# Performance work log

Hardware: AMD Instinct MI355X
Metric: run time of the kernel (lower is better)

Reference implementation:

```python
import jax, jax.numpy as jnp
import numpy as np
import math

B, S, D, H, FF = 32, 577, 768, 12, 3072
Dh = D // H
EPS = 1e-5


def layer_norm(x, w, b):
    mu = jnp.mean(x, axis=-1, keepdims=True)
    var = jnp.mean(jnp.square(x - mu), axis=-1, keepdims=True)
    return (x - mu) * jax.lax.rsqrt(var + EPS) * w + b


def setup_inputs() -> dict:
    key = jax.random.key(0)
    ks = jax.random.split(key, 12)
    s = 0.02
    return {
        "x": jax.random.normal(ks[0], (B, S, D), dtype=jnp.float32),
        "ln1_w": jnp.ones((D,), jnp.float32),
        "ln1_b": jnp.zeros((D,), jnp.float32),
        # stacked per-head Q/K/V projections (head order matches torch concat order)
        "Wq": jax.random.normal(ks[1], (H, D, Dh), jnp.float32) * s,
        "bq": jnp.zeros((H, Dh), jnp.float32),
        "Wk": jax.random.normal(ks[2], (H, D, Dh), jnp.float32) * s,
        "bk": jnp.zeros((H, Dh), jnp.float32),
        "Wv": jax.random.normal(ks[3], (H, D, Dh), jnp.float32) * s,
        "bv": jnp.zeros((H, Dh), jnp.float32),
        "Wo": jax.random.normal(ks[4], (D, D), jnp.float32) * s,
        "bo": jnp.zeros((D,), jnp.float32),
        "ln2_w": jnp.ones((D,), jnp.float32),
        "ln2_b": jnp.zeros((D,), jnp.float32),
        "W1": jax.random.normal(ks[5], (D, FF), jnp.float32) * s,
        "b1": jnp.zeros((FF,), jnp.float32),
        "W2": jax.random.normal(ks[6], (FF, D), jnp.float32) * s,
        "b2": jnp.zeros((D,), jnp.float32),
    }


def reference(x, ln1_w, ln1_b, Wq, bq, Wk, bk, Wv, bv, Wo, bo, ln2_w, ln2_b, W1, b1, W2, b2):
    # pre-norm attention
    h = layer_norm(x, ln1_w, ln1_b)  # [B,S,D]
    q = jnp.einsum('bsd,hde->bhse', h, Wq) + bq[:, None, :]
    k = jnp.einsum('bsd,hde->bhse', h, Wk) + bk[:, None, :]
    v = jnp.einsum('bsd,hde->bhse', h, Wv) + bv[:, None, :]
    scores = jnp.einsum('bhse,bhte->bhst', q, k) / math.sqrt(Dh)
    probs = jax.nn.softmax(scores, axis=-1)
    ctx = jnp.einsum('bhst,bhte->bhse', probs, v)  # [B,H,S,Dh]
    ctx = ctx.transpose(0, 2, 1, 3).reshape(B, S, H * Dh)  # concat heads
    attn_out = ctx @ Wo + bo
    x = x + attn_out
    # pre-norm MLP (exact GELU, as nn.GELU default)
    h2 = layer_norm(x, ln2_w, ln2_b)
    mlp = jax.nn.gelu(h2 @ W1 + b1, approximate=False) @ W2 + b2
    return x + mlp
```

## Files before the change

kernel.cpp:

```cpp
#include <hip/hip_runtime.h>
#include <hip/hip_bf16.h>
#include <stdint.h>

#define B_ 32
#define S_ 577
#define D_ 768
#define H_ 12
#define FF_ 3072
#define MROWS (B_*S_)

typedef __attribute__((ext_vector_type(8))) short sh8;
typedef __attribute__((ext_vector_type(4))) float f32x4;
typedef __attribute__((ext_vector_type(4))) unsigned short us4;

static __device__ __forceinline__ unsigned short f2b(float f) {
  __hip_bfloat16 h = __float2bfloat16(f);
  return *reinterpret_cast<unsigned short*>(&h);
}
static __device__ __forceinline__ float b2f(unsigned short u) {
  __hip_bfloat16 h;
  *reinterpret_cast<unsigned short*>(&h) = u;
  return __bfloat162float(h);
}

static __device__ __forceinline__ float fast_gelu(float v) {
  const float z = fabsf(v) * 0.70710678118f;
  const float t = __builtin_amdgcn_rcpf(__builtin_fmaf(0.3275911f, z, 1.0f));
  float p = 1.061405429f;
  p = __builtin_fmaf(p, t, -1.453152027f);
  p = __builtin_fmaf(p, t,  1.421413741f);
  p = __builtin_fmaf(p, t, -0.284496736f);
  p = __builtin_fmaf(p, t,  0.254829592f);
  p = p * t;
  const float e = __expf(-z * z);
  const float erf_abs = __builtin_fmaf(-p, e, 1.0f);
  const float erf_v = copysignf(erf_abs, v);
  const float hv = 0.5f * v;
  return __builtin_fmaf(hv, erf_v, hv);
}

#define GLOAD_LDS16(gp, lp) \
  __builtin_amdgcn_global_load_lds((const __attribute__((address_space(1))) unsigned int*)(gp), \
                                   (__attribute__((address_space(3))) unsigned int*)(lp), 16, 0, 0)

__global__ __launch_bounds__(256) void packT64(
    const float* __restrict__ src, unsigned short* __restrict__ dst, int K, int N)
{
  __shared__ unsigned short t[64][65];
  const int tid = threadIdx.x;
  const int c = tid & 63, r4 = tid >> 6;
  const int kb = blockIdx.y * 64, nb = blockIdx.x * 64;
#pragma unroll
  for (int p = 0; p < 16; ++p) {
    const int ko = p * 4 + r4;
    t[c][ko] = f2b(src[(size_t)(kb + ko) * N + nb + c]);
  }
  __syncthreads();
#pragma unroll
  for (int p = 0; p < 16; ++p) {
    const int rr = p * 4 + r4;
    dst[(size_t)(nb + rr) * K + kb + c] = t[rr][c];
  }
}

__global__ __launch_bounds__(256) void packQKV64(
    const float* __restrict__ Wq, const float* __restrict__ Wk, const float* __restrict__ Wv,
    unsigned short* __restrict__ dst)
{
  __shared__ unsigned short t[64][65];
  const int tid = threadIdx.x;
  const int c = tid & 63, r4 = tid >> 6;
  const int kb = blockIdx.x * 64;
  const int h = blockIdx.y;
  const int which = blockIdx.z;
  const float* src = ((which == 0) ? Wq : (which == 1) ? Wk : Wv) + (size_t)h * 768 * 64;
  const float scl = (which == 0) ? 0.125f : 1.0f;
#pragma unroll
  for (int p = 0; p < 16; ++p) {
    const int ko = p * 4 + r4;
    t[c][ko] = f2b(src[(size_t)(kb + ko) * 64 + c] * scl);
  }
  __syncthreads();
  unsigned short* db = dst + (size_t)(which * 768 + h * 64) * 768;
#pragma unroll
  for (int p = 0; p < 16; ++p) {
    const int rr = p * 4 + r4;
    db[(size_t)rr * 768 + kb + c] = t[rr][c];
  }
}

__global__ __launch_bounds__(256) void bias_pack(
    const float* __restrict__ bq, const float* __restrict__ bk, const float* __restrict__ bv,
    float* __restrict__ biasq)
{
  const int idx = blockIdx.x * 256 + threadIdx.x;
  if (idx < 2304) {
    const int wb = idx / 768, rb = idx - wb * 768;
    const float* bb = (wb == 0) ? bq : (wb == 1) ? bk : bv;
    biasq[idx] = bb[rb] * (wb == 0 ? 0.125f : 1.0f);
  }
}

__global__ __launch_bounds__(256) void ln_bf16(
    const float* __restrict__ x, const float* __restrict__ w, const float* __restrict__ bse,
    unsigned short* __restrict__ out)
{
  const int row = blockIdx.x;
  const int tid = threadIdx.x;
  const float* xr = x + (size_t)row * 768;
  float v0 = xr[tid], v1 = xr[tid + 256], v2 = xr[tid + 512];
  float s = v0 + v1 + v2;
  float ss = v0 * v0 + v1 * v1 + v2 * v2;
#pragma unroll
  for (int off = 32; off >= 1; off >>= 1) {
    s  += __shfl_xor(s, off);
    ss += __shfl_xor(ss, off);
  }
  __shared__ float red[8];
  const int wv = tid >> 6, ln = tid & 63;
  if (ln == 0) { red[wv] = s; red[wv + 4] = ss; }
  __syncthreads();
  s  = red[0] + red[1] + red[2] + red[3];
  ss = red[4] + red[5] + red[6] + red[7];
  const float mu = s * (1.f / 768.f);
  const float var = ss * (1.f / 768.f) - mu * mu;
  const float rs = rsqrtf(var + 1e-5f);
  unsigned short* orow = out + (size_t)row * 768;
  orow[tid]       = f2b((v0 - mu) * rs * w[tid]       + bse[tid]);
  orow[tid + 256] = f2b((v1 - mu) * rs * w[tid + 256] + bse[tid + 256]);
  orow[tid + 512] = f2b((v2 - mu) * rs * w[tid + 512] + bse[tid + 512]);
}

template<int EPI>
__global__ __launch_bounds__(256, 3) void gemm128(
    const unsigned short* __restrict__ A, const unsigned short* __restrict__ Bt,
    const float* __restrict__ bias, const float* __restrict__ res,
    unsigned short* __restrict__ obf, float* __restrict__ of32,
    int M, int N, int K)
{
  __shared__ __align__(16) unsigned short sAB[2][128 * 64];
  const int tid = threadIdx.x;
  const int wid = tid >> 6, ln = tid & 63;
  const int wr = wid >> 1, wc = wid & 1;
  const int l15 = ln & 15, lg = ln >> 4;
  const int l7 = l15 & 7;
  const int uo0 = ((lg) ^ l7) * 8;
  const int uo1 = ((4 + lg) ^ l7) * 8;
  const int srow = ln >> 3;
  const int scol = ((ln & 7) ^ srow) * 8;
  const int NT = K >> 6;

  const int gx = N >> 7;
  const int gm = (M + 127) >> 7;
  const int nwg = gridDim.x;
  const int q = nwg >> 3, r = nwg & 7;
  const int x = blockIdx.x & 7, ii = blockIdx.x >> 3;
  const int wg = (x < r ? x * (q + 1) : r * (q + 1) + (x - r) * q) + ii;
  int bm, bn;
  {
    const int g8 = gx >> 3, rem = gx & 7;
    const int per_full = gm << 3;
    if (wg < g8 * per_full) {
      const int bg = wg / per_full;
      const int r2 = wg - bg * per_full;
      bm = r2 >> 3; bn = (bg << 3) + (r2 & 7);
    } else {
      const int r2 = wg - g8 * per_full;
      bm = r2 / rem; bn = (g8 << 3) + (r2 - bm * rem);
    }
  }

  const int arow = wr * 64 + l15;
  const int brow = wc * 64 + l15;

  const unsigned short* ap0; const unsigned short* ap1;
  const unsigned short* ap2; const unsigned short* ap3;
  const unsigned short* bp0; const unsigned short* bp1;
  const unsigned short* bp2; const unsigned short* bp3;
  {
    int g0 = bm * 128 + (wid * 4 + 0) * 8 + srow; if (g0 >= M) g0 = M - 1;
    int g1 = bm * 128 + (wid * 4 + 1) * 8 + srow; if (g1 >= M) g1 = M - 1;
    int g2 = bm * 128 + (wid * 4 + 2) * 8 + srow; if (g2 >= M) g2 = M - 1;
    int g3 = bm * 128 + (wid * 4 + 3) * 8 + srow; if (g3 >= M) g3 = M - 1;
    ap0 = A + (size_t)g0 * K + scol; ap1 = A + (size_t)g1 * K + scol;
    ap2 = A + (size_t)g2 * K + scol; ap3 = A + (size_t)g3 * K + scol;
    const int b0 = bn * 128 + (wid * 4 + 0) * 8 + srow;
    bp0 = Bt + (size_t)b0 * K + scol;
    bp1 = bp0 + (size_t)8 * K; bp2 = bp0 + (size_t)16 * K; bp3 = bp0 + (size_t)24 * K;
  }
  unsigned short* const lA = sAB[0] + wid * 4 * 512;
  unsigned short* const lB = sAB[1] + wid * 4 * 512;

  f32x4 acc[4][4] = {};

  for (int t = 0; t < NT; ++t) {
    __syncthreads();
    GLOAD_LDS16(ap0, lA);        GLOAD_LDS16(ap1, lA + 512);
    GLOAD_LDS16(ap2, lA + 1024); GLOAD_LDS16(ap3, lA + 1536);
    GLOAD_LDS16(bp0, lB);        GLOAD_LDS16(bp1, lB + 512);
    GLOAD_LDS16(bp2, lB + 1024); GLOAD_LDS16(bp3, lB + 1536);
    ap0 += 64; ap1 += 64; ap2 += 64; ap3 += 64;
    bp0 += 64; bp1 += 64; bp2 += 64; bp3 += 64;
    asm volatile("s_waitcnt vmcnt(0)" ::: "memory");
    __syncthreads();

#pragma unroll
    for (int kk = 0; kk < 2; ++kk) {
      const int uo = kk ? uo1 : uo0;
      sh8 af[4], bf[4];
#pragma unroll
      for (int mi = 0; mi < 4; ++mi)
        af[mi] = *(const sh8*)(sAB[0] + (arow + mi * 16) * 64 + uo);
#pragma unroll
      for (int ni = 0; ni < 4; ++ni)
        bf[ni] = *(const sh8*)(sAB[1] + (brow + ni * 16) * 64 + uo);
#pragma unroll
      for (int mi = 0; mi < 4; ++mi)
#pragma unroll
        for (int ni = 0; ni < 4; ++ni)
          acc[mi][ni] = __builtin_amdgcn_mfma_f32_16x16x32_bf16(af[mi], bf[ni], acc[mi][ni], 0, 0, 0);
    }
  }

  constexpr int ESTR = 132;
  float* eps = (float*)sAB;
  const int ecol = (tid & 31) * 4;
  const int gcol = bn * 128 + ecol;
  const f32x4 bvh = *(const f32x4*)(bias + gcol);
  const int erow0 = tid >> 5;
#pragma unroll
  for (int pass = 0; pass < 4; ++pass) {
    __syncthreads();
    if (wr == (pass >> 1)) {
      const int mib = (pass & 1) * 2;
#pragma unroll
      for (int ml = 0; ml < 2; ++ml)
#pragma unroll
        for (int ni = 0; ni < 4; ++ni)
#pragma unroll
          for (int rr = 0; rr < 4; ++rr)
            eps[(ml * 16 + lg * 4 + rr) * ESTR + wc * 64 + ni * 16 + l15] = acc[mib + ml][ni][rr];
    }
    __syncthreads();
#pragma unroll
    for (int pp = 0; pp < 4; ++pp) {
      const int rl = pp * 8 + erow0;
      const int grow = bm * 128 + pass * 32 + rl;
      if (grow < M) {
        f32x4 v = *(const f32x4*)(eps + rl * ESTR + ecol);
        v += bvh;
        if (EPI == 2) {
#pragma unroll
          for (int e = 0; e < 4; ++e) v[e] = fast_gelu(v[e]);
        }
        if (EPI == 1) {
          const f32x4 rv = *(const f32x4*)(res + (size_t)grow * N + gcol);
          v += rv;
          *(f32x4*)(of32 + (size_t)grow * N + gcol) = v;
        } else {
          us4 o = { f2b(v[0]), f2b(v[1]), f2b(v[2]), f2b(v[3]) };
          *(us4*)(obf + (size_t)grow * N + gcol) = o;
        }
      }
    }
  }
}

__global__ __launch_bounds__(512) void attn(
    const unsigned short* __restrict__ qkv, unsigned short* __restrict__ ctx)
{
  constexpr int KP = 72;
  __shared__ __align__(16) unsigned short sQ[128 * KP];
  __shared__ __align__(16) unsigned short sK[64 * KP];
  __shared__ __align__(16) unsigned short sVT[64 * KP];
  __shared__ __align__(16) unsigned short sP[8][16 * KP];
  const int tid = threadIdx.x, wv = tid >> 6, ln = tid & 63;
  const int l15 = ln & 15, lg = ln >> 4;
  const int b = blockIdx.z, h = blockIdx.y, qt = blockIdx.x;
  const size_t base = (size_t)b * S_ * 2304 + h * 64;
  const unsigned short* qp = qkv + base;
  const unsigned short* kp = qkv + base + 768;
  const unsigned short* vp = qkv + base + 1536;

  {
    const int r = tid >> 2, c = (tid & 3) * 16;
    int row = qt * 128 + r; if (row >= S_) row = S_ - 1;
    const unsigned short* g = qp + (size_t)row * 2304 + c;
    *(sh8*)(sQ + r * KP + c)     = *(const sh8*)g;
    *(sh8*)(sQ + r * KP + c + 8) = *(const sh8*)(g + 8);
  }

  const int kr = tid >> 3, kc = (tid & 7) * 8;
  const unsigned short* krow = kp + (size_t)kr * 2304 + kc;
  unsigned short* const sKdst = sK + kr * KP + kc;
  const int ve = tid & 63, vkvb = tid >> 6;
  const unsigned short* vrow = vp + (size_t)vkvb * 8 * 2304 + ve;
  unsigned short* const sVdst = sVT + ve * KP + vkvb * 8;

  f32x4 oacc[4] = {};
  float m_run = -1e30f, l_run = 0.f;
  const int nt = (S_ + 63) / 64;
  for (int t = 0; t < nt; ++t) {
    __syncthreads();
    if (t < nt - 1) {
      *(sh8*)sKdst = *(const sh8*)krow;
      krow += (size_t)64 * 2304;
      {
        unsigned short val[8];
#pragma unroll
        for (int j = 0; j < 8; ++j) val[j] = vrow[(size_t)j * 2304];
        *(sh8*)sVdst = *(sh8*)val;
        vrow += (size_t)64 * 2304;
      }
    } else {
      {
        int row = t * 64 + kr; if (row >= S_) row = S_ - 1;
        *(sh8*)sKdst = *(const sh8*)(kp + (size_t)row * 2304 + kc);
      }
      {
        unsigned short val[8];
#pragma unroll
        for (int j = 0; j < 8; ++j) {
          int row = t * 64 + vkvb * 8 + j; if (row >= S_) row = S_ - 1;
          val[j] = vp[(size_t)row * 2304 + ve];
        }
        *(sh8*)sVdst = *(sh8*)val;
      }
    }
    __syncthreads();

    f32x4 sacc[4] = {};
#pragma unroll
    for (int kk = 0; kk < 2; ++kk) {
      sh8 bq = *(const sh8*)(sQ + (wv * 16 + l15) * KP + kk * 32 + lg * 8);
#pragma unroll
      for (int f = 0; f < 4; ++f) {
        sh8 ak = *(const sh8*)(sK + (f * 16 + l15) * KP + kk * 32 + lg * 8);
        sacc[f] = __builtin_amdgcn_mfma_f32_16x16x32_bf16(ak, bq, sacc[f], 0, 0, 0);
      }
    }

    if (t == nt - 1) {
#pragma unroll
      for (int f = 0; f < 4; ++f)
#pragma unroll
        for (int r = 0; r < 4; ++r)
          if (t * 64 + f * 16 + lg * 4 + r >= S_) sacc[f][r] = -1e30f;
    }
    float pmax = -1e30f;
#pragma unroll
    for (int f = 0; f < 4; ++f)
#pragma unroll
      for (int r = 0; r < 4; ++r) pmax = fmaxf(pmax, sacc[f][r]);
    pmax = fmaxf(pmax, __shfl_xor(pmax, 16));
    pmax = fmaxf(pmax, __shfl_xor(pmax, 32));
    const float mnew = fmaxf(m_run, pmax);
    const float alpha = __expf(m_run - mnew);
    float psum = 0.f;
    unsigned short pb[4][4];
#pragma unroll
    for (int f = 0; f < 4; ++f)
#pragma unroll
      for (int r = 0; r < 4; ++r) {
        const float p = __expf(sacc[f][r] - mnew);
        psum += p;
        pb[f][r] = f2b(p);
      }
    psum += __shfl_xor(psum, 16);
    psum += __shfl_xor(psum, 32);
    l_run = l_run * alpha + psum;
    m_run = mnew;
#pragma unroll
    for (int f = 0; f < 4; ++f) {
      oacc[f][0] *= alpha; oacc[f][1] *= alpha;
      oacc[f][2] *= alpha; oacc[f][3] *= alpha;
    }
#pragma unroll
    for (int f = 0; f < 4; ++f) {
      us4 pk = { pb[f][0], pb[f][1], pb[f][2], pb[f][3] };
      *(us4*)(sP[wv] + l15 * KP + f * 16 + lg * 4) = pk;
    }
    __syncthreads();

#pragma unroll
    for (int kk = 0; kk < 2; ++kk) {
      sh8 bp = *(const sh8*)(sP[wv] + l15 * KP + kk * 32 + lg * 8);
#pragma unroll
      for (int fe = 0; fe < 4; ++fe) {
        sh8 av = *(const sh8*)(sVT + (fe * 16 + l15) * KP + kk * 32 + lg * 8);
        oacc[fe] = __builtin_amdgcn_mfma_f32_16x16x32_bf16(av, bp, oacc[fe], 0, 0, 0);
      }
    }
  }

  const int qa = qt * 128 + wv * 16 + l15;
  if (qa < S_) {
    const float inv = 1.f / l_run;
    const size_t orow = ((size_t)b * S_ + qa) * 768 + h * 64;
#pragma unroll
    for (int fe = 0; fe < 4; ++fe) {
      unsigned short pk[4];
#pragma unroll
      for (int r = 0; r < 4; ++r) pk[r] = f2b(oacc[fe][r] * inv);
      *(us4*)(ctx + orow + fe * 16 + lg * 4) = *(us4*)pk;
    }
  }
}

extern "C" void kernel_launch(void* const* d_in, const int* in_sizes, int n_in,
                              void* d_out, int out_size, void* d_ws, size_t ws_size,
                              hipStream_t stream)
{
  const float* x    = (const float*)d_in[0];
  const float* ln1w = (const float*)d_in[1];
  const float* ln1b = (const float*)d_in[2];
  const float* Wq   = (const float*)d_in[3];
  const float* bq   = (const float*)d_in[4];
  const float* Wk   = (const float*)d_in[5];
  const float* bk   = (const float*)d_in[6];
  const float* Wv   = (const float*)d_in[7];
  const float* bv   = (const float*)d_in[8];
  const float* Wo   = (const float*)d_in[9];
  const float* bo   = (const float*)d_in[10];
  const float* ln2w = (const float*)d_in[11];
  const float* ln2b = (const float*)d_in[12];
  const float* W1   = (const float*)d_in[13];
  const float* b1   = (const float*)d_in[14];
  const float* W2   = (const float*)d_in[15];
  const float* b2   = (const float*)d_in[16];
  float* out = (float*)d_out;
  char* ws = (char*)d_ws;

  unsigned short* wqkvT = (unsigned short*)(ws + 0);
  unsigned short* woT   = (unsigned short*)(ws + 3538944);
  unsigned short* w1T   = (unsigned short*)(ws + 4718592);
  unsigned short* w2T   = (unsigned short*)(ws + 9437184);
  float*          biasq = (float*)(ws + 14155776);
  unsigned short* hbf   = (unsigned short*)(ws + 14164992);
  unsigned short* qkvb  = (unsigned short*)(ws + 42525696);
  unsigned short* ctxb  = (unsigned short*)(ws + 127607808);
  unsigned short* mlp1  = qkvb;

  packQKV64<<<dim3(12, 12, 3), 256, 0, stream>>>(Wq, Wk, Wv, wqkvT);
  bias_pack<<<9, 256, 0, stream>>>(bq, bk, bv, biasq);
  packT64<<<dim3(12, 12), 256, 0, stream>>>(Wo, woT, 768, 768);
  packT64<<<dim3(48, 12), 256, 0, stream>>>(W1, w1T, 768, 3072);
  packT64<<<dim3(12, 48), 256, 0, stream>>>(W2, w2T, 3072, 768);

  ln_bf16<<<MROWS, 256, 0, stream>>>(x, ln1w, ln1b, hbf);
  gemm128<0><<<145 * 18, 256, 0, stream>>>(hbf, wqkvT, biasq, nullptr, qkvb, nullptr,
                                           MROWS, 2304, 768);
  attn<<<dim3(5, 12, 32), 512, 0, stream>>>(qkvb, ctxb);
  gemm128<1><<<145 * 6, 256, 0, stream>>>(ctxb, woT, bo, x, nullptr, out,
                                          MROWS, 768, 768);
  ln_bf16<<<MROWS, 256, 0, stream>>>(out, ln2w, ln2b, hbf);
  gemm128<2><<<145 * 24, 256, 0, stream>>>(hbf, w1T, b1, nullptr, mlp1, nullptr,
                                           MROWS, 3072, 768);
  gemm128<1><<<145 * 6, 256, 0, stream>>>(mlp1, w2T, b2, out, nullptr, out,
                                          MROWS, 768, 3072);
}
```

Baseline: 474.5 us.

## Merge weight-pack launches into one kernel and vectorize layernorm

```diff
diff --git a/kernel.cpp b/kernel.cpp
--- a/kernel.cpp
+++ b/kernel.cpp
@@ -43,17 +43,16 @@
   __builtin_amdgcn_global_load_lds((const __attribute__((address_space(1))) unsigned int*)(gp), \
                                    (__attribute__((address_space(3))) unsigned int*)(lp), 16, 0, 0)
 
-__global__ __launch_bounds__(256) void packT64(
-    const float* __restrict__ src, unsigned short* __restrict__ dst, int K, int N)
+static __device__ __forceinline__ void packT_body(
+    const float* __restrict__ src, unsigned short* __restrict__ dst,
+    int K, int N, int kb, int nb, float scl, int tid)
 {
   __shared__ unsigned short t[64][65];
-  const int tid = threadIdx.x;
   const int c = tid & 63, r4 = tid >> 6;
-  const int kb = blockIdx.y * 64, nb = blockIdx.x * 64;
 #pragma unroll
   for (int p = 0; p < 16; ++p) {
     const int ko = p * 4 + r4;
-    t[c][ko] = f2b(src[(size_t)(kb + ko) * N + nb + c]);
+    t[c][ko] = f2b(src[(size_t)(kb + ko) * N + nb + c] * scl);
   }
   __syncthreads();
 #pragma unroll
@@ -63,72 +62,72 @@
   }
 }
 
-__global__ __launch_bounds__(256) void packQKV64(
-    const float* __restrict__ Wq, const float* __restrict__ Wk, const float* __restrict__ Wv,
-    unsigned short* __restrict__ dst)
-{
-  __shared__ unsigned short t[64][65];
+__global__ __launch_bounds__(256) void pack_all(
+    const float* __restrict__ Wq, const float* __restrict__ Wk,
+    const float* __restrict__ Wv, const float* __restrict__ Wo,
+    const float* __restrict__ W1, const float* __restrict__ W2,
+    const float* __restrict__ bq, const float* __restrict__ bk,
+    const float* __restrict__ bv,
+    unsigned short* __restrict__ wqkvT, unsigned short* __restrict__ woT,
+    unsigned short* __restrict__ w1T, unsigned short* __restrict__ w2T,
+    float* __restrict__ biasq)
+{
+  const int b = blockIdx.x;
   const int tid = threadIdx.x;
-  const int c = tid & 63, r4 = tid >> 6;
-  const int kb = blockIdx.x * 64;
-  const int h = blockIdx.y;
-  const int which = blockIdx.z;
-  const float* src = ((which == 0) ? Wq : (which == 1) ? Wk : Wv) + (size_t)h * 768 * 64;
-  const float scl = (which == 0) ? 0.125f : 1.0f;
-#pragma unroll
-  for (int p = 0; p < 16; ++p) {
-    const int ko = p * 4 + r4;
-    t[c][ko] = f2b(src[(size_t)(kb + ko) * 64 + c] * scl);
-  }
-  __syncthreads();
-  unsigned short* db = dst + (size_t)(which * 768 + h * 64) * 768;
-#pragma unroll
-  for (int p = 0; p < 16; ++p) {
-    const int rr = p * 4 + r4;
-    db[(size_t)rr * 768 + kb + c] = t[rr][c];
-  }
-}
-
-__global__ __launch_bounds__(256) void bias_pack(
-    const float* __restrict__ bq, const float* __restrict__ bk, const float* __restrict__ bv,
-    float* __restrict__ biasq)
-{
-  const int idx = blockIdx.x * 256 + threadIdx.x;
-  if (idx < 2304) {
-    const int wb = idx / 768, rb = idx - wb * 768;
-    const float* bb = (wb == 0) ? bq : (wb == 1) ? bk : bv;
-    biasq[idx] = bb[rb] * (wb == 0 ? 0.125f : 1.0f);
-  }
-}
-
-__global__ __launch_bounds__(256) void ln_bf16(
+  if (b < 144) {
+    packT_body(Wo, woT, 768, 768, (b / 12) * 64, (b % 12) * 64, 1.f, tid);
+  } else if (b < 720) {
+    const int i = b - 144;
+    packT_body(W1, w1T, 768, 3072, (i / 48) * 64, (i % 48) * 64, 1.f, tid);
+  } else if (b < 1296) {
+    const int i = b - 720;
+    packT_body(W2, w2T, 3072, 768, (i / 12) * 64, (i % 12) * 64, 1.f, tid);
+  } else if (b < 1728) {
+    const int i = b - 1296;
+    const int kb = i % 12, h = (i / 12) % 12, which = i / 144;
+    const float* src = ((which == 0) ? Wq : (which == 1) ? Wk : Wv) + (size_t)h * 768 * 64;
+    unsigned short* db = wqkvT + (size_t)(which * 768 + h * 64) * 768;
+    packT_body(src, db, 768, 64, kb * 64, 0, which == 0 ? 0.125f : 1.f, tid);
+  } else {
+    const int idx = (b - 1728) * 256 + tid;
+    if (idx < 2304) {
+      const int wb = idx / 768, rb = idx - wb * 768;
+      const float* bb = (wb == 0) ? bq : (wb == 1) ? bk : bv;
+      biasq[idx] = bb[rb] * (wb == 0 ? 0.125f : 1.f);
+    }
+  }
+}
+
+__global__ __launch_bounds__(192) void ln_bf16(
     const float* __restrict__ x, const float* __restrict__ w, const float* __restrict__ bse,
     unsigned short* __restrict__ out)
 {
   const int row = blockIdx.x;
   const int tid = threadIdx.x;
   const float* xr = x + (size_t)row * 768;
-  float v0 = xr[tid], v1 = xr[tid + 256], v2 = xr[tid + 512];
-  float s = v0 + v1 + v2;
-  float ss = v0 * v0 + v1 * v1 + v2 * v2;
+  const f32x4 v = *(const f32x4*)(xr + tid * 4);
+  float s  = v[0] + v[1] + v[2] + v[3];
+  float ss = v[0]*v[0] + v[1]*v[1] + v[2]*v[2] + v[3]*v[3];
 #pragma unroll
   for (int off = 32; off >= 1; off >>= 1) {
     s  += __shfl_xor(s, off);
     ss += __shfl_xor(ss, off);
   }
-  __shared__ float red[8];
+  __shared__ float red[6];
   const int wv = tid >> 6, ln = tid & 63;
-  if (ln == 0) { red[wv] = s; red[wv + 4] = ss; }
+  if (ln == 0) { red[wv] = s; red[wv + 3] = ss; }
   __syncthreads();
-  s  = red[0] + red[1] + red[2] + red[3];
-  ss = red[4] + red[5] + red[6] + red[7];
+  s  = red[0] + red[1] + red[2];
+  ss = red[3] + red[4] + red[5];
   const float mu = s * (1.f / 768.f);
   const float var = ss * (1.f / 768.f) - mu * mu;
   const float rs = rsqrtf(var + 1e-5f);
-  unsigned short* orow = out + (size_t)row * 768;
-  orow[tid]       = f2b((v0 - mu) * rs * w[tid]       + bse[tid]);
-  orow[tid + 256] = f2b((v1 - mu) * rs * w[tid + 256] + bse[tid + 256]);
-  orow[tid + 512] = f2b((v2 - mu) * rs * w[tid + 512] + bse[tid + 512]);
+  const f32x4 w4 = *(const f32x4*)(w + tid * 4);
+  const f32x4 b4 = *(const f32x4*)(bse + tid * 4);
+  us4 o;
+#pragma unroll
+  for (int e = 0; e < 4; ++e) o[e] = f2b((v[e] - mu) * rs * w4[e] + b4[e]);
+  *(us4*)(out + (size_t)row * 768 + tid * 4) = o;
 }
 
 template<int EPI>
@@ -173,20 +172,14 @@
   const int arow = wr * 64 + l15;
   const int brow = wc * 64 + l15;
 
-  const unsigned short* ap0; const unsigned short* ap1;
-  const unsigned short* ap2; const unsigned short* ap3;
-  const unsigned short* bp0; const unsigned short* bp1;
-  const unsigned short* bp2; const unsigned short* bp3;
-  {
-    int g0 = bm * 128 + (wid * 4 + 0) * 8 + srow; if (g0 >= M) g0 = M - 1;
-    int g1 = bm * 128 + (wid * 4 + 1) * 8 + srow; if (g1 >= M) g1 = M - 1;
-    int g2 = bm * 128 + (wid * 4 + 2) * 8 + srow; if (g2 >= M) g2 = M - 1;
-    int g3 = bm * 128 + (wid * 4 + 3) * 8 + srow; if (g3 >= M) g3 = M - 1;
-    ap0 = A + (size_t)g0 * K + scol; ap1 = A + (size_t)g1 * K + scol;
-    ap2 = A + (size_t)g2 * K + scol; ap3 = A + (size_t)g3 * K + scol;
-    const int b0 = bn * 128 + (wid * 4 + 0) * 8 + srow;
-    bp0 = Bt + (size_t)b0 * K + scol;
-    bp1 = bp0 + (size_t)8 * K; bp2 = bp0 + (size_t)16 * K; bp3 = bp0 + (size_t)24 * K;
+  const unsigned short* ap[4];
+  const unsigned short* bp[4];
+#pragma unroll
+  for (int j = 0; j < 4; ++j) {
+    int ga = bm * 128 + (wid * 4 + j) * 8 + srow; if (ga >= M) ga = M - 1;
+    ap[j] = A + (size_t)ga * K + scol;
+    const int gb = bn * 128 + (wid * 4 + j) * 8 + srow;
+    bp[j] = Bt + (size_t)gb * K + scol;
   }
   unsigned short* const lA = sAB[0] + wid * 4 * 512;
   unsigned short* const lB = sAB[1] + wid * 4 * 512;
@@ -195,12 +188,10 @@
 
   for (int t = 0; t < NT; ++t) {
     __syncthreads();
-    GLOAD_LDS16(ap0, lA);        GLOAD_LDS16(ap1, lA + 512);
-    GLOAD_LDS16(ap2, lA + 1024); GLOAD_LDS16(ap3, lA + 1536);
-    GLOAD_LDS16(bp0, lB);        GLOAD_LDS16(bp1, lB + 512);
-    GLOAD_LDS16(bp2, lB + 1024); GLOAD_LDS16(bp3, lB + 1536);
-    ap0 += 64; ap1 += 64; ap2 += 64; ap3 += 64;
-    bp0 += 64; bp1 += 64; bp2 += 64; bp3 += 64;
+#pragma unroll
+    for (int j = 0; j < 4; ++j) { GLOAD_LDS16(ap[j], lA + j * 512); ap[j] += 64; }
+#pragma unroll
+    for (int j = 0; j < 4; ++j) { GLOAD_LDS16(bp[j], lB + j * 512); bp[j] += 64; }
     asm volatile("s_waitcnt vmcnt(0)" ::: "memory");
     __syncthreads();
 
@@ -441,19 +432,16 @@
   unsigned short* ctxb  = (unsigned short*)(ws + 127607808);
   unsigned short* mlp1  = qkvb;
 
-  packQKV64<<<dim3(12, 12, 3), 256, 0, stream>>>(Wq, Wk, Wv, wqkvT);
-  bias_pack<<<9, 256, 0, stream>>>(bq, bk, bv, biasq);
-  packT64<<<dim3(12, 12), 256, 0, stream>>>(Wo, woT, 768, 768);
-  packT64<<<dim3(48, 12), 256, 0, stream>>>(W1, w1T, 768, 3072);
-  packT64<<<dim3(12, 48), 256, 0, stream>>>(W2, w2T, 3072, 768);
-
-  ln_bf16<<<MROWS, 256, 0, stream>>>(x, ln1w, ln1b, hbf);
+  pack_all<<<1737, 256, 0, stream>>>(Wq, Wk, Wv, Wo, W1, W2, bq, bk, bv,
+                                     wqkvT, woT, w1T, w2T, biasq);
+
+  ln_bf16<<<MROWS, 192, 0, stream>>>(x, ln1w, ln1b, hbf);
   gemm128<0><<<145 * 18, 256, 0, stream>>>(hbf, wqkvT, biasq, nullptr, qkvb, nullptr,
                                            MROWS, 2304, 768);
   attn<<<dim3(5, 12, 32), 512, 0, stream>>>(qkvb, ctxb);
   gemm128<1><<<145 * 6, 256, 0, stream>>>(ctxb, woT, bo, x, nullptr, out,
                                           MROWS, 768, 768);
-  ln_bf16<<<MROWS, 256, 0, stream>>>(out, ln2w, ln2b, hbf);
+  ln_bf16<<<MROWS, 192, 0, stream>>>(out, ln2w, ln2b, hbf);
   gemm128<2><<<145 * 24, 256, 0, stream>>>(hbf, w1T, b1, nullptr, mlp1, nullptr,
                                            MROWS, 3072, 768);
   gemm128<1><<<145 * 6, 256, 0, stream>>>(mlp1, w2T, b2, out, nullptr, out,
```

Measured after the change: 465.1 us. -2.0%, faster.
